# Kernel tuning notes

Hardware: AMD Instinct MI355X
Metric: run time of the kernel (lower is better)

Reference implementation:

```python
import jax, jax.numpy as jnp
import numpy as np
import math

B, L, M = 8, 1024, 1024
H, D, DK, DFF = 16, 1024, 64, 4096
EPS = 1e-5


def _ln(x, g, b):
    mu = jnp.mean(x, axis=-1, keepdims=True)
    var = jnp.mean((x - mu) ** 2, axis=-1, keepdims=True)
    return (x - mu) * jax.lax.rsqrt(var + EPS) * g + b


def _mha(x, kv, Wq, bq, Wk, bk, Wv, bv, Wo, bo, masked):
    # x: [B,Lq,D], kv: [B,Lk,D]; per-head weights stacked: Wq [H,D,DK], bq [H,DK]
    Q = jnp.einsum('bld,hdk->bhlk', x, Wq) + bq[None, :, None, :]
    K = jnp.einsum('bld,hdk->bhlk', kv, Wk) + bk[None, :, None, :]
    V = jnp.einsum('bld,hdk->bhlk', kv, Wv) + bv[None, :, None, :]
    scores = jnp.einsum('bhqk,bhmk->bhqm', Q, K) / math.sqrt(DK)
    p = jax.nn.softmax(scores, axis=-1)
    if masked:
        # faithful to source: mask applied AFTER softmax (multiply by tril ones)
        Lq = x.shape[1]
        tril = jnp.tril(jnp.ones((Lq, kv.shape[1]), dtype=p.dtype))
        p = p * tril
    z = jnp.einsum('bhqm,bhmk->bhqk', p, V)  # [B,H,Lq,DK]
    z = jnp.transpose(z, (0, 2, 1, 3)).reshape(x.shape[0], x.shape[1], H * DK)
    return z @ Wo + bo


def _forward(x, enc, Wq1, bq1, Wk1, bk1, Wv1, bv1, Wo1, bo1,
             Wq2, bq2, Wk2, bk2, Wv2, bv2, Wo2, bo2,
             W1, b1, W2, b2, g1, be1, g2, be2, g3, be3):
    z = _mha(x, x, Wq1, bq1, Wk1, bk1, Wv1, bv1, Wo1, bo1, masked=True)
    x = _ln(z + x, g1, be1)
    z = _mha(x, enc, Wq2, bq2, Wk2, bk2, Wv2, bv2, Wo2, bo2, masked=False)
    x = _ln(z + x, g2, be2)
    # Conv1d(k=1) pair == per-token MLP: relu(x @ W1 + b1) @ W2 + b2
    y = jax.nn.relu(x @ W1 + b1) @ W2 + b2
    return _ln(y + x, g3, be3)


def setup_inputs() -> dict:
    key = jax.random.key(0)
    ks = jax.random.split(key, 16)
    s = 0.02
    return {
        'x': jax.random.normal(ks[0], (B, L, D), jnp.float32),
        'enc': jax.random.normal(ks[1], (B, M, D), jnp.float32),
        'Wq1': jax.random.normal(ks[2], (H, D, DK), jnp.float32) * s,
        'bq1': jnp.zeros((H, DK), jnp.float32),
        'Wk1': jax.random.normal(ks[3], (H, D, DK), jnp.float32) * s,
        'bk1': jnp.zeros((H, DK), jnp.float32),
        'Wv1': jax.random.normal(ks[4], (H, D, DK), jnp.float32) * s,
        'bv1': jnp.zeros((H, DK), jnp.float32),
        'Wo1': jax.random.normal(ks[5], (H * DK, D), jnp.float32) * s,
        'bo1': jnp.zeros((D,), jnp.float32),
        'Wq2': jax.random.normal(ks[6], (H, D, DK), jnp.float32) * s,
        'bq2': jnp.zeros((H, DK), jnp.float32),
        'Wk2': jax.random.normal(ks[7], (H, D, DK), jnp.float32) * s,
        'bk2': jnp.zeros((H, DK), jnp.float32),
        'Wv2': jax.random.normal(ks[8], (H, D, DK), jnp.float32) * s,
        'bv2': jnp.zeros((H, DK), jnp.float32),
        'Wo2': jax.random.normal(ks[9], (H * DK, D), jnp.float32) * s,
        'bo2': jnp.zeros((D,), jnp.float32),
        'W1': jax.random.normal(ks[10], (D, DFF), jnp.float32) * s,
        'b1': jnp.zeros((DFF,), jnp.float32),
        'W2': jax.random.normal(ks[11], (DFF, D), jnp.float32) * s,
        'b2': jnp.zeros((D,), jnp.float32),
        'g1': jnp.ones((D,), jnp.float32), 'be1': jnp.zeros((D,), jnp.float32),
        'g2': jnp.ones((D,), jnp.float32), 'be2': jnp.zeros((D,), jnp.float32),
        'g3': jnp.ones((D,), jnp.float32), 'be3': jnp.zeros((D,), jnp.float32),
    }


def reference(x, enc, Wq1, bq1, Wk1, bk1, Wv1, bv1, Wo1, bo1,
              Wq2, bq2, Wk2, bk2, Wv2, bv2, Wo2, bo2,
              W1, b1, W2, b2, g1, be1, g2, be2, g3, be3):
    return _forward(x, enc, Wq1, bq1, Wk1, bk1, Wv1, bv1, Wo1, bo1,
                    Wq2, bq2, Wk2, bk2, Wv2, bv2, Wo2, bo2,
                    W1, b1, W2, b2, g1, be1, g2, be2, g3, be3)
```

## Files before the change

kernel.cpp:

```cpp
#include <hip/hip_runtime.h>
#include <hip/hip_bf16.h>

typedef __bf16 bf16;
typedef __bf16 bf16x8 __attribute__((ext_vector_type(8)));
typedef __bf16 bf16x4v __attribute__((ext_vector_type(4)));
typedef float f32x4 __attribute__((ext_vector_type(4)));
typedef unsigned int u32;
typedef u32 u32x4 __attribute__((ext_vector_type(4)));

#define DEV static __device__ __forceinline__

DEV void gll16(const void* g, void* l) {
  __builtin_amdgcn_global_load_lds((__attribute__((address_space(1))) void*)g,
                                   (__attribute__((address_space(3))) void*)l,
                                   16, 0, 0);
}

DEV bf16 tobf(float f) { return (bf16)f; }

DEV u32 cvtpk(float lo, float hi) {
  u32 r;
  asm("v_cvt_pk_bf16_f32 %0, %1, %2" : "=v"(r) : "v"(lo), "v"(hi));
  return r;
}

__global__ void cast_f2b_kernel(const float* __restrict__ in, bf16* __restrict__ out, int n4) {
  int i = blockIdx.x * 256 + threadIdx.x;
  if (i < n4) {
    const float4 v = ((const float4*)in)[i];
    bf16x4v o;
    o[0] = tobf(v.x); o[1] = tobf(v.y); o[2] = tobf(v.z); o[3] = tobf(v.w);
    ((bf16x4v*)out)[i] = o;
  }
}

__global__ __launch_bounds__(256)
void tpack_kernel(const float* __restrict__ in, bf16* __restrict__ out,
                  int K, int N, int in_hs, int out_hs, float scale) {
  __shared__ float tile[32][33];
  const int k0 = blockIdx.x << 5, n0 = blockIdx.y << 5;
  const float* ip = in + (size_t)blockIdx.z * in_hs;
  bf16* op = out + (size_t)blockIdx.z * out_hs;
  const int tx = threadIdx.x & 31, ty = threadIdx.x >> 5;
#pragma unroll
  for (int r = 0; r < 4; ++r)
    tile[ty * 4 + r][tx] = ip[(size_t)(k0 + ty * 4 + r) * N + n0 + tx];
  __syncthreads();
#pragma unroll
  for (int r = 0; r < 4; ++r)
    op[(size_t)(n0 + ty * 4 + r) * K + k0 + tx] = tobf(tile[tx][ty * 4 + r] * scale);
}

__global__ void bscale_kernel(const float* __restrict__ in, float* __restrict__ out, int n, float s) {
  int i = blockIdx.x * 256 + threadIdx.x;
  if (i < n) out[i] = in[i] * s;
}

template<int EPI>
__global__ __launch_bounds__(512, 2)
void gemm8(const bf16* __restrict__ A, const bf16* __restrict__ W,
           const float* __restrict__ bias, const float* __restrict__ resid,
           void* __restrict__ outv, int M, int N, int K) {
  __shared__ bf16 sA[3][256 * 64];
  __shared__ bf16 sB[3][128 * 64];
  const int nbx = N >> 7;
  const int nwg = (M >> 8) * nbx;
  int bid = (int)blockIdx.x;
  bid = (bid & 7) * (nwg >> 3) + (bid >> 3);
  const int tm = bid / nbx, tn = bid - tm * nbx;
  const int tid = threadIdx.x;
  const int lane = tid & 63;
  const int w = tid >> 6;
  const int wr = w >> 1, wc = w & 1;
  const int l15 = lane & 15, l4 = lane >> 4;

  const bf16* Abase = A + (size_t)(tm * 256) * K;
  const bf16* Bbase = W + (size_t)(tn * 128) * K;

  f32x4 acc[4][4] = {};
  const int nt = K >> 6;

  auto stageA = [&](int buf, int t) {
#pragma unroll
    for (int j = 0; j < 4; ++j) {
      int g = tid + (j << 9);
      int row = g >> 3;
      int sc = ((g & 7) ^ (row & 7)) << 3;
      gll16(Abase + (size_t)row * K + (t << 6) + sc, &sA[buf][g << 3]);
    }
  };
  auto stageB = [&](int buf, int t) {
#pragma unroll
    for (int j = 0; j < 2; ++j) {
      int g = tid + (j << 9);
      int row = g >> 3;
      int sc = ((g & 7) ^ (row & 7)) << 3;
      gll16(Bbase + (size_t)row * K + (t << 6) + sc, &sB[buf][g << 3]);
    }
  };

  stageA(0, 0); stageB(0, 0);
  stageA(1, 1 < nt ? 1 : 0); stageB(1, 1 < nt ? 1 : 0);
  __builtin_amdgcn_sched_barrier(0);
  asm volatile("s_waitcnt vmcnt(6)" ::: "memory");
  __builtin_amdgcn_s_barrier();

  int c = 0;
  for (int t = 0; t < nt; ++t) {
    const int sb = (c >= 1) ? c - 1 : 2;
    const int ts = (t + 2 < nt) ? t + 2 : nt - 1;
    bf16x8 af[4][2], bfr[4][2];
#pragma unroll
    for (int mi = 0; mi < 4; ++mi)
#pragma unroll
      for (int kk = 0; kk < 2; ++kk) {
        int r = wr * 64 + (mi << 4) + l15;
        int off = (r << 7) + (kk << 6) + (l4 << 4);
        off ^= (r & 7) << 4;
        af[mi][kk] = *(const bf16x8*)((const char*)sA[c] + off);
      }
#pragma unroll
    for (int ni = 0; ni < 2; ++ni)
#pragma unroll
      for (int kk = 0; kk < 2; ++kk) {
        int r = wc * 64 + (ni << 4) + l15;
        int off = (r << 7) + (kk << 6) + (l4 << 4);
        off ^= (r & 7) << 4;
        bfr[ni][kk] = *(const bf16x8*)((const char*)sB[c] + off);
      }
    stageA(sb, ts);
    __builtin_amdgcn_sched_barrier(0);
    __builtin_amdgcn_s_barrier();
    asm volatile("s_waitcnt lgkmcnt(0)" ::: "memory");
    __builtin_amdgcn_sched_barrier(0);
    __builtin_amdgcn_s_setprio(1);
#pragma unroll
    for (int mi = 0; mi < 4; ++mi)
#pragma unroll
      for (int ni = 0; ni < 2; ++ni)
#pragma unroll
        for (int kk = 0; kk < 2; ++kk)
          acc[mi][ni] = __builtin_amdgcn_mfma_f32_16x16x32_bf16(af[mi][kk], bfr[ni][kk],
                                                                acc[mi][ni], 0, 0, 0);
    __builtin_amdgcn_s_setprio(0);
    __builtin_amdgcn_sched_barrier(0);
    __builtin_amdgcn_s_barrier();
#pragma unroll
    for (int ni = 2; ni < 4; ++ni)
#pragma unroll
      for (int kk = 0; kk < 2; ++kk) {
        int r = wc * 64 + (ni << 4) + l15;
        int off = (r << 7) + (kk << 6) + (l4 << 4);
        off ^= (r & 7) << 4;
        bfr[ni][kk] = *(const bf16x8*)((const char*)sB[c] + off);
      }
    stageB(sb, ts);
    __builtin_amdgcn_sched_barrier(0);
    asm volatile("s_waitcnt vmcnt(6)" ::: "memory");
    __builtin_amdgcn_s_barrier();
    asm volatile("s_waitcnt lgkmcnt(0)" ::: "memory");
    __builtin_amdgcn_sched_barrier(0);
    __builtin_amdgcn_s_setprio(1);
#pragma unroll
    for (int mi = 0; mi < 4; ++mi)
#pragma unroll
      for (int ni = 2; ni < 4; ++ni)
#pragma unroll
        for (int kk = 0; kk < 2; ++kk)
          acc[mi][ni] = __builtin_amdgcn_mfma_f32_16x16x32_bf16(af[mi][kk], bfr[ni][kk],
                                                                acc[mi][ni], 0, 0, 0);
    __builtin_amdgcn_s_setprio(0);
    __builtin_amdgcn_sched_barrier(0);
    __builtin_amdgcn_s_barrier();
    c = (c == 2) ? 0 : c + 1;
  }

  const int row0 = tm * 256 + wr * 64 + (l4 << 2);
  const int col0 = tn * 128 + wc * 64 + l15;
#pragma unroll
  for (int ni = 0; ni < 4; ++ni) {
    const int col = col0 + (ni << 4);
    const float bv = bias ? bias[col] : 0.f;
#pragma unroll
    for (int mi = 0; mi < 4; ++mi) {
      const int rr = row0 + (mi << 4);
      f32x4 v = acc[mi][ni];
      if (EPI == 0) {
        bf16* out = (bf16*)outv;
#pragma unroll
        for (int r = 0; r < 4; ++r) out[(size_t)(rr + r) * N + col] = tobf(v[r] + bv);
      } else if (EPI == 1) {
        float* out = (float*)outv;
#pragma unroll
        for (int r = 0; r < 4; ++r) {
          size_t idx = (size_t)(rr + r) * N + col;
          out[idx] = v[r] + bv + resid[idx];
        }
      } else if (EPI == 2) {
        bf16* out = (bf16*)outv;
#pragma unroll
        for (int r = 0; r < 4; ++r) out[(size_t)(rr + r) * N + col] = tobf(fmaxf(v[r] + bv, 0.f));
      } else if (EPI == 3) {
        bf16* out = (bf16*)outv;
        const int bb = rr >> 10, l0 = rr & 1023;
        const int hh = col >> 6, dk = col & 63;
        bf16x4v pk;
#pragma unroll
        for (int r = 0; r < 4; ++r) pk[r] = tobf(v[r] + bv);
        *(bf16x4v*)(out + ((size_t)((bb * 16 + hh) * 64 + dk) << 10) + l0) = pk;
      } else {
        bf16* out = (bf16*)outv;
        const int seg = col >> 10;
        const int cc = col & 1023;
        const bool isV = (EPI == 4) ? (seg == 2) : (seg == 1);
        if (isV) {
          bf16* vout = out + (size_t)seg * 8388608;
          const int bb = rr >> 10, l0 = rr & 1023;
          const int hh = cc >> 6, dk = cc & 63;
          bf16x4v pk;
#pragma unroll
          for (int r = 0; r < 4; ++r) pk[r] = tobf(v[r] + bv);
          *(bf16x4v*)(vout + ((size_t)((bb * 16 + hh) * 64 + dk) << 10) + l0) = pk;
        } else {
          bf16* qout = out + (size_t)seg * 8388608;
#pragma unroll
          for (int r = 0; r < 4; ++r) qout[(size_t)(rr + r) * 1024 + cc] = tobf(v[r] + bv);
        }
      }
    }
  }
}

template<bool MASKED>
__global__ __launch_bounds__(256, 2)
void attn_kernel(const bf16* __restrict__ Qp, const bf16* __restrict__ Kp,
                 const bf16* __restrict__ Vt, bf16* __restrict__ Z) {
  __shared__ bf16 sK[2][64 * 64];
  __shared__ bf16 sV[2][64 * 64];
  const int Lk = 1024;
  const int d = blockIdx.x;
  const int bh = d & 127, qb = d >> 7;
  const int b = bh >> 4, h = bh & 15;
  const int q0 = qb << 7;
  const int tid = threadIdx.x, lane = tid & 63, w = tid >> 6;
  const int l15 = lane & 15, l4 = lane >> 4;

  const bf16* Qb = Qp + ((size_t)(b * 1024 + q0 + w * 32)) * 1024 + h * 64;
  bf16x8 qf[2][2];
#pragma unroll
  for (int mi = 0; mi < 2; ++mi)
#pragma unroll
    for (int kk = 0; kk < 2; ++kk)
      qf[mi][kk] = *(const bf16x8*)(Qb + (size_t)((mi << 4) + l15) * 1024 + (kk << 5) + (l4 << 3));

  f32x4 o[4][2] = {};
  float Mr[2] = {-1e30f, -1e30f}, LrP[2] = {0.f, 0.f};

  const bf16* Kb = Kp + ((size_t)b * Lk) * 1024 + h * 64;
  const bf16* Vb = Vt + ((size_t)(b * 16 + h)) * 64 * Lk;

  auto stage = [&](int buf, int t, bool withV) {
    const int kv0 = t << 6;
#pragma unroll
    for (int j = 0; j < 2; ++j) {
      int g = tid + (j << 8);
      int r = g >> 3;
      int sc = ((g & 7) ^ (r & 7)) << 3;
      gll16(Kb + (size_t)(kv0 + r) * 1024 + sc, &sK[buf][g << 3]);
      if (withV) gll16(Vb + (size_t)r * Lk + kv0 + sc, &sV[buf][g << 3]);
    }
  };
  auto needPV = [&](int t) -> bool { return !MASKED || ((t << 6) < q0 + 128); };

  const int NT = Lk >> 6;
  stage(0, 0, true);
  __syncthreads();
  int cur = 0;

  for (int t = 0; t < NT; ++t) {
    if (t + 1 < NT) stage(cur ^ 1, t + 1, needPV(t + 1));
    const int kv0 = t << 6;

    f32x4 s[4][2] = {};
#pragma unroll
    for (int n = 0; n < 4; ++n) {
      bf16x8 kf[2];
#pragma unroll
      for (int kk = 0; kk < 2; ++kk) {
        int r = (n << 4) + l15;
        int off = (r << 7) + (kk << 6) + (l4 << 4);
        off ^= (r & 7) << 4;
        kf[kk] = *(const bf16x8*)((const char*)sK[cur] + off);
      }
#pragma unroll
      for (int mi = 0; mi < 2; ++mi)
#pragma unroll
        for (int kk = 0; kk < 2; ++kk)
          s[n][mi] = __builtin_amdgcn_mfma_f32_16x16x32_bf16(kf[kk], qf[mi][kk],
                                                             s[n][mi], 0, 0, 0);
    }

#pragma unroll
    for (int mi = 0; mi < 2; ++mi) {
      float lmax = s[0][mi][0];
#pragma unroll
      for (int n = 0; n < 4; ++n)
#pragma unroll
        for (int r = 0; r < 4; ++r) lmax = fmaxf(lmax, s[n][mi][r]);
      const bool need = (t == 0) || !__all(lmax <= Mr[mi] + 8.f);
      if (need) {
        float tmx = fmaxf(lmax, __shfl_xor(lmax, 16, 64));
        tmx = fmaxf(tmx, __shfl_xor(tmx, 32, 64));
        const float Mn = fmaxf(Mr[mi], tmx);
        const float al = exp2f(Mr[mi] - Mn);
        LrP[mi] *= al;
        Mr[mi] = Mn;
#pragma unroll
        for (int r = 0; r < 4; ++r) {
          float a = __shfl(al, (l4 << 2) + r, 64);
#pragma unroll
          for (int nd = 0; nd < 4; ++nd) o[nd][mi][r] *= a;
        }
      }
      float rs = 0.f;
#pragma unroll
      for (int n = 0; n < 4; ++n)
#pragma unroll
        for (int r = 0; r < 4; ++r) {
          float p = exp2f(s[n][mi][r] - Mr[mi]);
          s[n][mi][r] = p;
          rs += p;
        }
      LrP[mi] += rs;
    }

    if (needPV(t)) {
      const bool needMask = MASKED && (kv0 + 63 > q0 + (w << 5));
      bf16x8 pa[2][2];
#pragma unroll
      for (int mi = 0; mi < 2; ++mi) {
        u32 D0[4], D1[4];
        const int qg = q0 + (w << 5) + (mi << 4) + l15;
#pragma unroll
        for (int n = 0; n < 4; ++n) {
          float pv[4];
#pragma unroll
          for (int r = 0; r < 4; ++r) {
            float p = s[n][mi][r];
            if (needMask) {
              int cg = kv0 + (n << 4) + (l4 << 2) + r;
              if (cg > qg) p = 0.f;
            }
            pv[r] = p;
          }
          D0[n] = cvtpk(pv[0], pv[1]);
          D1[n] = cvtpk(pv[2], pv[3]);
        }
        const int src = l15 + ((lane & 16) << 1);
#pragma unroll
        for (int kk = 0; kk < 2; ++kk) {
          u32 v0 = (lane & 32) ? D0[2 * kk + 1] : D0[2 * kk];
          u32 v1 = (lane & 32) ? D1[2 * kk + 1] : D1[2 * kk];
          u32x4 tw;
          tw[0] = (u32)__shfl((int)v0, src, 64);
          tw[1] = (u32)__shfl((int)v1, src, 64);
          tw[2] = (u32)__shfl((int)v0, src + 16, 64);
          tw[3] = (u32)__shfl((int)v1, src + 16, 64);
          pa[mi][kk] = __builtin_bit_cast(bf16x8, tw);
        }
      }
#pragma unroll
      for (int nd = 0; nd < 4; ++nd) {
        bf16x8 vf[2];
#pragma unroll
        for (int kk = 0; kk < 2; ++kk) {
          int r = (nd << 4) + l15;
          int off = (r << 7) + (kk << 6) + (l4 << 4);
          off ^= (r & 7) << 4;
          vf[kk] = *(const bf16x8*)((const char*)sV[cur] + off);
        }
#pragma unroll
        for (int mi = 0; mi < 2; ++mi)
#pragma unroll
          for (int kk = 0; kk < 2; ++kk)
            o[nd][mi] = __builtin_amdgcn_mfma_f32_16x16x32_bf16(pa[mi][kk], vf[kk],
                                                                o[nd][mi], 0, 0, 0);
      }
    }
    __syncthreads();
    cur ^= 1;
  }

  float inv[2][4];
#pragma unroll
  for (int mi = 0; mi < 2; ++mi) {
    float l = LrP[mi];
    l += __shfl_xor(l, 16, 64);
    l += __shfl_xor(l, 32, 64);
    const float il = 1.f / l;
#pragma unroll
    for (int r = 0; r < 4; ++r) inv[mi][r] = __shfl(il, (l4 << 2) + r, 64);
  }
  bf16* Zb = Z + ((size_t)(b * 1024 + q0 + w * 32)) * 1024 + h * 64;
#pragma unroll
  for (int nd = 0; nd < 4; ++nd)
#pragma unroll
    for (int mi = 0; mi < 2; ++mi)
#pragma unroll
      for (int r = 0; r < 4; ++r)
        Zb[(size_t)((mi << 4) + (l4 << 2) + r) * 1024 + (nd << 4) + l15] =
            tobf(o[nd][mi][r] * inv[mi][r]);
}

__global__ __launch_bounds__(256)
void ln_kernel(const float* __restrict__ in, const float* __restrict__ gw,
               const float* __restrict__ bw, float* __restrict__ outf,
               bf16* __restrict__ outb) {
  const int row = blockIdx.x, tid = threadIdx.x;
  const size_t base = (size_t)row << 10;
  const float4 v = *(const float4*)(in + base + tid * 4);
  float s = v.x + v.y + v.z + v.w;
  float ss = v.x * v.x + v.y * v.y + v.z * v.z + v.w * v.w;
#pragma unroll
  for (int d = 1; d < 64; d <<= 1) { s += __shfl_xor(s, d, 64); ss += __shfl_xor(ss, d, 64); }
  __shared__ float red[8];
  const int w = tid >> 6;
  if ((tid & 63) == 0) { red[w] = s; red[4 + w] = ss; }
  __syncthreads();
  s = red[0] + red[1] + red[2] + red[3];
  ss = red[4] + red[5] + red[6] + red[7];
  const float mu = s * (1.f / 1024.f);
  const float var = ss * (1.f / 1024.f) - mu * mu;
  const float rstd = rsqrtf(var + 1e-5f);
  const float4 g4 = *(const float4*)(gw + tid * 4);
  const float4 b4 = *(const float4*)(bw + tid * 4);
  const float o0 = (v.x - mu) * rstd * g4.x + b4.x;
  const float o1 = (v.y - mu) * rstd * g4.y + b4.y;
  const float o2 = (v.z - mu) * rstd * g4.z + b4.z;
  const float o3 = (v.w - mu) * rstd * g4.w + b4.w;
  if (outf) { float4 of; of.x = o0; of.y = o1; of.z = o2; of.w = o3;
              *(float4*)(outf + base + tid * 4) = of; }
  if (outb) { bf16x4v ob; ob[0] = tobf(o0); ob[1] = tobf(o1); ob[2] = tobf(o2); ob[3] = tobf(o3);
              *(bf16x4v*)(outb + base + tid * 4) = ob; }
}

extern "C" void kernel_launch(void* const* d_in, const int* in_sizes, int n_in,
                              void* d_out, int out_size, void* d_ws, size_t ws_size,
                              hipStream_t stream) {
  const float* x   = (const float*)d_in[0];
  const float* enc = (const float*)d_in[1];
  const float* Wq1 = (const float*)d_in[2];
  const float* bq1 = (const float*)d_in[3];
  const float* Wk1 = (const float*)d_in[4];
  const float* bk1 = (const float*)d_in[5];
  const float* Wv1 = (const float*)d_in[6];
  const float* bv1 = (const float*)d_in[7];
  const float* Wo1 = (const float*)d_in[8];
  const float* bo1 = (const float*)d_in[9];
  const float* Wq2 = (const float*)d_in[10];
  const float* bq2 = (const float*)d_in[11];
  const float* Wk2 = (const float*)d_in[12];
  const float* bk2 = (const float*)d_in[13];
  const float* Wv2 = (const float*)d_in[14];
  const float* bv2 = (const float*)d_in[15];
  const float* Wo2 = (const float*)d_in[16];
  const float* bo2 = (const float*)d_in[17];
  const float* W1  = (const float*)d_in[18];
  const float* b1  = (const float*)d_in[19];
  const float* W2  = (const float*)d_in[20];
  const float* b2  = (const float*)d_in[21];
  const float* g1  = (const float*)d_in[22];
  const float* be1 = (const float*)d_in[23];
  const float* g2  = (const float*)d_in[24];
  const float* be2 = (const float*)d_in[25];
  const float* g3  = (const float*)d_in[26];
  const float* be3 = (const float*)d_in[27];

  char* ws = (char*)d_ws;
  size_t off = 0;
  auto alloc = [&](size_t bytes) { char* p = ws + off; off += (bytes + 255) & ~(size_t)255; return p; };
  const size_t ACT = (size_t)8 * 1024 * 1024 * 2;
  const float QSC = 0.125f * 1.44269504088896f;

  bf16* xb     = (bf16*)alloc(ACT);
  bf16* encb   = (bf16*)alloc(ACT);
  bf16* Wqkv1t = (bf16*)alloc((size_t)3072 * 1024 * 2);
  bf16* Wkv2t  = (bf16*)alloc((size_t)2048 * 1024 * 2);
  bf16* Wq2t   = (bf16*)alloc((size_t)1024 * 1024 * 2);
  bf16* Wo1t   = (bf16*)alloc((size_t)1024 * 1024 * 2);
  bf16* Wo2t   = (bf16*)alloc((size_t)1024 * 1024 * 2);
  bf16* W1t    = (bf16*)alloc((size_t)4096 * 1024 * 2);
  bf16* W2t    = (bf16*)alloc((size_t)4096 * 1024 * 2);
  float* qkvb1 = (float*)alloc(3072 * 4);
  float* kvb2  = (float*)alloc(2048 * 4);
  float* sbq2  = (float*)alloc(1024 * 4);
  char*  S     = alloc((size_t)64 * 1024 * 1024);
  float* rbuf  = (float*)alloc((size_t)8 * 1024 * 1024 * 4);
  float* xnf   = (float*)alloc((size_t)8 * 1024 * 1024 * 4);
  bf16*  xnb   = (bf16*)alloc(ACT);

  bf16* q1   = (bf16*)(S);
  bf16* k1   = (bf16*)(S + ACT);
  bf16* vt1  = (bf16*)(S + 2 * ACT);
  bf16* z1   = (bf16*)(S + 3 * ACT);
  bf16* hbuf = (bf16*)S;

  dim3 b256(256);
  dim3 b512(512);
  cast_f2b_kernel<<<8192, b256, 0, stream>>>(x, xb, 2097152);
  cast_f2b_kernel<<<8192, b256, 0, stream>>>(enc, encb, 2097152);
  tpack_kernel<<<dim3(32, 2, 16), b256, 0, stream>>>(Wq1, Wqkv1t, 1024, 64, 65536, 65536, QSC);
  tpack_kernel<<<dim3(32, 2, 16), b256, 0, stream>>>(Wk1, Wqkv1t + 1048576, 1024, 64, 65536, 65536, 1.f);
  tpack_kernel<<<dim3(32, 2, 16), b256, 0, stream>>>(Wv1, Wqkv1t + 2097152, 1024, 64, 65536, 65536, 1.f);
  tpack_kernel<<<dim3(32, 2, 16), b256, 0, stream>>>(Wq2, Wq2t, 1024, 64, 65536, 65536, QSC);
  tpack_kernel<<<dim3(32, 2, 16), b256, 0, stream>>>(Wk2, Wkv2t, 1024, 64, 65536, 65536, 1.f);
  tpack_kernel<<<dim3(32, 2, 16), b256, 0, stream>>>(Wv2, Wkv2t + 1048576, 1024, 64, 65536, 65536, 1.f);
  tpack_kernel<<<dim3(32, 32, 1), b256, 0, stream>>>(Wo1, Wo1t, 1024, 1024, 0, 0, 1.f);
  tpack_kernel<<<dim3(32, 32, 1), b256, 0, stream>>>(Wo2, Wo2t, 1024, 1024, 0, 0, 1.f);
  tpack_kernel<<<dim3(32, 128, 1), b256, 0, stream>>>(W1, W1t, 1024, 4096, 0, 0, 1.f);
  tpack_kernel<<<dim3(128, 32, 1), b256, 0, stream>>>(W2, W2t, 4096, 1024, 0, 0, 1.f);
  bscale_kernel<<<4, b256, 0, stream>>>(bq1, qkvb1, 1024, QSC);
  bscale_kernel<<<4, b256, 0, stream>>>(bk1, qkvb1 + 1024, 1024, 1.f);
  bscale_kernel<<<4, b256, 0, stream>>>(bv1, qkvb1 + 2048, 1024, 1.f);
  bscale_kernel<<<4, b256, 0, stream>>>(bk2, kvb2, 1024, 1.f);
  bscale_kernel<<<4, b256, 0, stream>>>(bv2, kvb2 + 1024, 1024, 1.f);
  bscale_kernel<<<4, b256, 0, stream>>>(bq2, sbq2, 1024, QSC);

  gemm8<4><<<768, b512, 0, stream>>>(xb, Wqkv1t, qkvb1, nullptr, q1, 8192, 3072, 1024);
  attn_kernel<true><<<1024, b256, 0, stream>>>(q1, k1, vt1, z1);
  gemm8<1><<<256, b512, 0, stream>>>(z1, Wo1t, bo1, x, rbuf, 8192, 1024, 1024);
  ln_kernel<<<8192, b256, 0, stream>>>(rbuf, g1, be1, xnf, xnb);

  gemm8<0><<<256, b512, 0, stream>>>(xnb, Wq2t, sbq2, nullptr, q1, 8192, 1024, 1024);
  gemm8<5><<<512, b512, 0, stream>>>(encb, Wkv2t, kvb2, nullptr, k1, 8192, 2048, 1024);
  attn_kernel<false><<<1024, b256, 0, stream>>>(q1, k1, vt1, z1);
  gemm8<1><<<256, b512, 0, stream>>>(z1, Wo2t, bo2, xnf, rbuf, 8192, 1024, 1024);
  ln_kernel<<<8192, b256, 0, stream>>>(rbuf, g2, be2, xnf, xnb);

  gemm8<2><<<1024, b512, 0, stream>>>(xnb, W1t, b1, nullptr, hbuf, 8192, 4096, 1024);
  gemm8<1><<<256, b512, 0, stream>>>(hbuf, W2t, b2, xnf, rbuf, 8192, 1024, 4096);
  ln_kernel<<<8192, b256, 0, stream>>>(rbuf, g3, be3, (float*)d_out, nullptr);
}
```

Measured before the change: 603.3 us.

## Compute V projections as transposed GEMMs and group GEMM tiles for locality

```diff
diff --git a/kernel.cpp b/kernel.cpp
--- a/kernel.cpp
+++ b/kernel.cpp
@@ -9,6 +9,11 @@
 typedef u32 u32x4 __attribute__((ext_vector_type(4)));
 
 #define DEV static __device__ __forceinline__
+#define SB0 __builtin_amdgcn_sched_barrier(0)
+#define BAR __builtin_amdgcn_s_barrier()
+#define LGKM0 asm volatile("s_waitcnt lgkmcnt(0)" ::: "memory")
+#define PRIO1 __builtin_amdgcn_s_setprio(1)
+#define PRIO0 __builtin_amdgcn_s_setprio(0)
 
 DEV void gll16(const void* g, void* l) {
   __builtin_amdgcn_global_load_lds((__attribute__((address_space(1))) void*)g,
@@ -56,8 +61,20 @@
   if (i < n) out[i] = in[i] * s;
 }
 
+DEV void tile_map(int bid, int nwg, int nbx, int& tm, int& tn) {
+  bid = (bid & 7) * (nwg >> 3) + (bid >> 3);
+  const int gid = bid >> 4, g4 = bid & 15;
+  const int gpr = nbx >> 2;
+  tm = ((gid / gpr) << 2) | (g4 >> 2);
+  tn = ((gid % gpr) << 2) | (g4 & 3);
+}
+
+DEV int lane_base(int l15, int l4, int kk) {
+  return (l15 << 7) + (((kk << 6) | (l4 << 4)) ^ ((l15 & 7) << 4));
+}
+
 template<int EPI>
-__global__ __launch_bounds__(512, 2)
+__global__ __launch_bounds__(512, 1)
 void gemm8(const bf16* __restrict__ A, const bf16* __restrict__ W,
            const float* __restrict__ bias, const float* __restrict__ resid,
            void* __restrict__ outv, int M, int N, int K) {
@@ -65,9 +82,8 @@
   __shared__ bf16 sB[3][128 * 64];
   const int nbx = N >> 7;
   const int nwg = (M >> 8) * nbx;
-  int bid = (int)blockIdx.x;
-  bid = (bid & 7) * (nwg >> 3) + (bid >> 3);
-  const int tm = bid / nbx, tn = bid - tm * nbx;
+  int tm, tn;
+  tile_map((int)blockIdx.x, nwg, nbx, tm, tn);
   const int tid = threadIdx.x;
   const int lane = tid & 63;
   const int w = tid >> 6;
@@ -77,63 +93,74 @@
   const bf16* Abase = A + (size_t)(tm * 256) * K;
   const bf16* Bbase = W + (size_t)(tn * 128) * K;
 
+  const bf16* gAsrc[4];
+  int loffA[4];
+#pragma unroll
+  for (int j = 0; j < 4; ++j) {
+    int g = tid + (j << 9);
+    int row = g >> 3;
+    int sc = ((g & 7) ^ (row & 7)) << 3;
+    gAsrc[j] = Abase + (size_t)row * K + sc;
+    loffA[j] = g << 4;
+  }
+  const bf16* gBsrc[2];
+  int loffB[2];
+#pragma unroll
+  for (int j = 0; j < 2; ++j) {
+    int g = tid + (j << 9);
+    int row = g >> 3;
+    int sc = ((g & 7) ^ (row & 7)) << 3;
+    gBsrc[j] = Bbase + (size_t)row * K + sc;
+    loffB[j] = g << 4;
+  }
+
+  int obA[2], obB[2];
+#pragma unroll
+  for (int kk = 0; kk < 2; ++kk) {
+    obA[kk] = wr * 8192 + lane_base(l15, l4, kk);
+    obB[kk] = wc * 8192 + lane_base(l15, l4, kk);
+  }
+
   f32x4 acc[4][4] = {};
   const int nt = K >> 6;
 
   auto stageA = [&](int buf, int t) {
-#pragma unroll
-    for (int j = 0; j < 4; ++j) {
-      int g = tid + (j << 9);
-      int row = g >> 3;
-      int sc = ((g & 7) ^ (row & 7)) << 3;
-      gll16(Abase + (size_t)row * K + (t << 6) + sc, &sA[buf][g << 3]);
-    }
+    const int db = buf << 15;
+    const size_t so = (size_t)t << 6;
+#pragma unroll
+    for (int j = 0; j < 4; ++j) gll16(gAsrc[j] + so, (char*)sA + db + loffA[j]);
   };
   auto stageB = [&](int buf, int t) {
-#pragma unroll
-    for (int j = 0; j < 2; ++j) {
-      int g = tid + (j << 9);
-      int row = g >> 3;
-      int sc = ((g & 7) ^ (row & 7)) << 3;
-      gll16(Bbase + (size_t)row * K + (t << 6) + sc, &sB[buf][g << 3]);
-    }
+    const int db = buf << 14;
+    const size_t so = (size_t)t << 6;
+#pragma unroll
+    for (int j = 0; j < 2; ++j) gll16(gBsrc[j] + so, (char*)sB + db + loffB[j]);
   };
 
   stageA(0, 0); stageB(0, 0);
   stageA(1, 1 < nt ? 1 : 0); stageB(1, 1 < nt ? 1 : 0);
-  __builtin_amdgcn_sched_barrier(0);
+  SB0;
   asm volatile("s_waitcnt vmcnt(6)" ::: "memory");
-  __builtin_amdgcn_s_barrier();
+  BAR;
 
   int c = 0;
   for (int t = 0; t < nt; ++t) {
     const int sb = (c >= 1) ? c - 1 : 2;
     const int ts = (t + 2 < nt) ? t + 2 : nt - 1;
+    const int aOff = c << 15, bOff = c << 14;
     bf16x8 af[4][2], bfr[4][2];
 #pragma unroll
     for (int mi = 0; mi < 4; ++mi)
 #pragma unroll
-      for (int kk = 0; kk < 2; ++kk) {
-        int r = wr * 64 + (mi << 4) + l15;
-        int off = (r << 7) + (kk << 6) + (l4 << 4);
-        off ^= (r & 7) << 4;
-        af[mi][kk] = *(const bf16x8*)((const char*)sA[c] + off);
-      }
+      for (int kk = 0; kk < 2; ++kk)
+        af[mi][kk] = *(const bf16x8*)((const char*)sA + aOff + obA[kk] + (mi << 11));
 #pragma unroll
     for (int ni = 0; ni < 2; ++ni)
 #pragma unroll
-      for (int kk = 0; kk < 2; ++kk) {
-        int r = wc * 64 + (ni << 4) + l15;
-        int off = (r << 7) + (kk << 6) + (l4 << 4);
-        off ^= (r & 7) << 4;
-        bfr[ni][kk] = *(const bf16x8*)((const char*)sB[c] + off);
-      }
+      for (int kk = 0; kk < 2; ++kk)
+        bfr[ni][kk] = *(const bf16x8*)((const char*)sB + bOff + obB[kk] + (ni << 11));
     stageA(sb, ts);
-    __builtin_amdgcn_sched_barrier(0);
-    __builtin_amdgcn_s_barrier();
-    asm volatile("s_waitcnt lgkmcnt(0)" ::: "memory");
-    __builtin_amdgcn_sched_barrier(0);
-    __builtin_amdgcn_s_setprio(1);
+    SB0; BAR; LGKM0; SB0; PRIO1;
 #pragma unroll
     for (int mi = 0; mi < 4; ++mi)
 #pragma unroll
@@ -142,25 +169,16 @@
         for (int kk = 0; kk < 2; ++kk)
           acc[mi][ni] = __builtin_amdgcn_mfma_f32_16x16x32_bf16(af[mi][kk], bfr[ni][kk],
                                                                 acc[mi][ni], 0, 0, 0);
-    __builtin_amdgcn_s_setprio(0);
-    __builtin_amdgcn_sched_barrier(0);
-    __builtin_amdgcn_s_barrier();
+    PRIO0; SB0; BAR;
 #pragma unroll
     for (int ni = 2; ni < 4; ++ni)
 #pragma unroll
-      for (int kk = 0; kk < 2; ++kk) {
-        int r = wc * 64 + (ni << 4) + l15;
-        int off = (r << 7) + (kk << 6) + (l4 << 4);
-        off ^= (r & 7) << 4;
-        bfr[ni][kk] = *(const bf16x8*)((const char*)sB[c] + off);
-      }
+      for (int kk = 0; kk < 2; ++kk)
+        bfr[ni][kk] = *(const bf16x8*)((const char*)sB + bOff + obB[kk] + (ni << 11));
     stageB(sb, ts);
-    __builtin_amdgcn_sched_barrier(0);
+    SB0;
     asm volatile("s_waitcnt vmcnt(6)" ::: "memory");
-    __builtin_amdgcn_s_barrier();
-    asm volatile("s_waitcnt lgkmcnt(0)" ::: "memory");
-    __builtin_amdgcn_sched_barrier(0);
-    __builtin_amdgcn_s_setprio(1);
+    BAR; LGKM0; SB0; PRIO1;
 #pragma unroll
     for (int mi = 0; mi < 4; ++mi)
 #pragma unroll
@@ -169,9 +187,7 @@
         for (int kk = 0; kk < 2; ++kk)
           acc[mi][ni] = __builtin_amdgcn_mfma_f32_16x16x32_bf16(af[mi][kk], bfr[ni][kk],
                                                                 acc[mi][ni], 0, 0, 0);
-    __builtin_amdgcn_s_setprio(0);
-    __builtin_amdgcn_sched_barrier(0);
-    __builtin_amdgcn_s_barrier();
+    PRIO0; SB0; BAR;
     c = (c == 2) ? 0 : c + 1;
   }
 
@@ -180,7 +196,7 @@
 #pragma unroll
   for (int ni = 0; ni < 4; ++ni) {
     const int col = col0 + (ni << 4);
-    const float bv = bias ? bias[col] : 0.f;
+    const float bv = (EPI == 6) ? 0.f : bias[col];
 #pragma unroll
     for (int mi = 0; mi < 4; ++mi) {
       const int rr = row0 + (mi << 4);
@@ -200,32 +216,19 @@
         bf16* out = (bf16*)outv;
 #pragma unroll
         for (int r = 0; r < 4; ++r) out[(size_t)(rr + r) * N + col] = tobf(fmaxf(v[r] + bv, 0.f));
-      } else if (EPI == 3) {
-        bf16* out = (bf16*)outv;
-        const int bb = rr >> 10, l0 = rr & 1023;
-        const int hh = col >> 6, dk = col & 63;
-        bf16x4v pk;
-#pragma unroll
-        for (int r = 0; r < 4; ++r) pk[r] = tobf(v[r] + bv);
-        *(bf16x4v*)(out + ((size_t)((bb * 16 + hh) * 64 + dk) << 10) + l0) = pk;
-      } else {
+      } else if (EPI == 4) {
         bf16* out = (bf16*)outv;
         const int seg = col >> 10;
         const int cc = col & 1023;
-        const bool isV = (EPI == 4) ? (seg == 2) : (seg == 1);
-        if (isV) {
-          bf16* vout = out + (size_t)seg * 8388608;
-          const int bb = rr >> 10, l0 = rr & 1023;
-          const int hh = cc >> 6, dk = cc & 63;
-          bf16x4v pk;
-#pragma unroll
-          for (int r = 0; r < 4; ++r) pk[r] = tobf(v[r] + bv);
-          *(bf16x4v*)(vout + ((size_t)((bb * 16 + hh) * 64 + dk) << 10) + l0) = pk;
-        } else {
-          bf16* qout = out + (size_t)seg * 8388608;
-#pragma unroll
-          for (int r = 0; r < 4; ++r) qout[(size_t)(rr + r) * 1024 + cc] = tobf(v[r] + bv);
-        }
+        bf16* qout = out + (size_t)seg * 8388608;
+#pragma unroll
+        for (int r = 0; r < 4; ++r) qout[(size_t)(rr + r) * 1024 + cc] = tobf(v[r] + bv);
+      } else {
+        bf16* out = (bf16*)outv;
+        const float4 bq = *(const float4*)(bias + rr);
+        const float br[4] = {bq.x, bq.y, bq.z, bq.w};
+#pragma unroll
+        for (int r = 0; r < 4; ++r) out[(size_t)(rr + r) * N + col] = tobf(v[r] + br[r]);
       }
     }
   }
@@ -257,7 +260,7 @@
   float Mr[2] = {-1e30f, -1e30f}, LrP[2] = {0.f, 0.f};
 
   const bf16* Kb = Kp + ((size_t)b * Lk) * 1024 + h * 64;
-  const bf16* Vb = Vt + ((size_t)(b * 16 + h)) * 64 * Lk;
+  const bf16* Vb = Vt + (size_t)(h * 64) * 8192 + b * 1024;
 
   auto stage = [&](int buf, int t, bool withV) {
     const int kv0 = t << 6;
@@ -267,7 +270,7 @@
       int r = g >> 3;
       int sc = ((g & 7) ^ (r & 7)) << 3;
       gll16(Kb + (size_t)(kv0 + r) * 1024 + sc, &sK[buf][g << 3]);
-      if (withV) gll16(Vb + (size_t)r * Lk + kv0 + sc, &sV[buf][g << 3]);
+      if (withV) gll16(Vb + (size_t)r * 8192 + kv0 + sc, &sV[buf][g << 3]);
     }
   };
   auto needPV = [&](int t) -> bool { return !MASKED || ((t << 6) < q0 + 128); };
@@ -484,15 +487,16 @@
 
   bf16* xb     = (bf16*)alloc(ACT);
   bf16* encb   = (bf16*)alloc(ACT);
-  bf16* Wqkv1t = (bf16*)alloc((size_t)3072 * 1024 * 2);
-  bf16* Wkv2t  = (bf16*)alloc((size_t)2048 * 1024 * 2);
+  bf16* Wqk1t  = (bf16*)alloc((size_t)2048 * 1024 * 2);
+  bf16* Wv1t   = (bf16*)alloc((size_t)1024 * 1024 * 2);
   bf16* Wq2t   = (bf16*)alloc((size_t)1024 * 1024 * 2);
+  bf16* Wk2t   = (bf16*)alloc((size_t)1024 * 1024 * 2);
+  bf16* Wv2t   = (bf16*)alloc((size_t)1024 * 1024 * 2);
   bf16* Wo1t   = (bf16*)alloc((size_t)1024 * 1024 * 2);
   bf16* Wo2t   = (bf16*)alloc((size_t)1024 * 1024 * 2);
   bf16* W1t    = (bf16*)alloc((size_t)4096 * 1024 * 2);
   bf16* W2t    = (bf16*)alloc((size_t)4096 * 1024 * 2);
-  float* qkvb1 = (float*)alloc(3072 * 4);
-  float* kvb2  = (float*)alloc(2048 * 4);
+  float* qkb1  = (float*)alloc(2048 * 4);
   float* sbq2  = (float*)alloc(1024 * 4);
   char*  S     = alloc((size_t)64 * 1024 * 1024);
   float* rbuf  = (float*)alloc((size_t)8 * 1024 * 1024 * 4);
@@ -509,30 +513,29 @@
   dim3 b512(512);
   cast_f2b_kernel<<<8192, b256, 0, stream>>>(x, xb, 2097152);
   cast_f2b_kernel<<<8192, b256, 0, stream>>>(enc, encb, 2097152);
-  tpack_kernel<<<dim3(32, 2, 16), b256, 0, stream>>>(Wq1, Wqkv1t, 1024, 64, 65536, 65536, QSC);
-  tpack_kernel<<<dim3(32, 2, 16), b256, 0, stream>>>(Wk1, Wqkv1t + 1048576, 1024, 64, 65536, 65536, 1.f);
-  tpack_kernel<<<dim3(32, 2, 16), b256, 0, stream>>>(Wv1, Wqkv1t + 2097152, 1024, 64, 65536, 65536, 1.f);
+  tpack_kernel<<<dim3(32, 2, 16), b256, 0, stream>>>(Wq1, Wqk1t, 1024, 64, 65536, 65536, QSC);
+  tpack_kernel<<<dim3(32, 2, 16), b256, 0, stream>>>(Wk1, Wqk1t + 1048576, 1024, 64, 65536, 65536, 1.f);
+  tpack_kernel<<<dim3(32, 2, 16), b256, 0, stream>>>(Wv1, Wv1t, 1024, 64, 65536, 65536, 1.f);
   tpack_kernel<<<dim3(32, 2, 16), b256, 0, stream>>>(Wq2, Wq2t, 1024, 64, 65536, 65536, QSC);
-  tpack_kernel<<<dim3(32, 2, 16), b256, 0, stream>>>(Wk2, Wkv2t, 1024, 64, 65536, 65536, 1.f);
-  tpack_kernel<<<dim3(32, 2, 16), b256, 0, stream>>>(Wv2, Wkv2t + 1048576, 1024, 64, 65536, 65536, 1.f);
+  tpack_kernel<<<dim3(32, 2, 16), b256, 0, stream>>>(Wk2, Wk2t, 1024, 64, 65536, 65536, 1.f);
+  tpack_kernel<<<dim3(32, 2, 16), b256, 0, stream>>>(Wv2, Wv2t, 1024, 64, 65536, 65536, 1.f);
   tpack_kernel<<<dim3(32, 32, 1), b256, 0, stream>>>(Wo1, Wo1t, 1024, 1024, 0, 0, 1.f);
   tpack_kernel<<<dim3(32, 32, 1), b256, 0, stream>>>(Wo2, Wo2t, 1024, 1024, 0, 0, 1.f);
   tpack_kernel<<<dim3(32, 128, 1), b256, 0, stream>>>(W1, W1t, 1024, 4096, 0, 0, 1.f);
   tpack_kernel<<<dim3(128, 32, 1), b256, 0, stream>>>(W2, W2t, 4096, 1024, 0, 0, 1.f);
-  bscale_kernel<<<4, b256, 0, stream>>>(bq1, qkvb1, 1024, QSC);
-  bscale_kernel<<<4, b256, 0, stream>>>(bk1, qkvb1 + 1024, 1024, 1.f);
-  bscale_kernel<<<4, b256, 0, stream>>>(bv1, qkvb1 + 2048, 1024, 1.f);
-  bscale_kernel<<<4, b256, 0, stream>>>(bk2, kvb2, 1024, 1.f);
-  bscale_kernel<<<4, b256, 0, stream>>>(bv2, kvb2 + 1024, 1024, 1.f);
+  bscale_kernel<<<4, b256, 0, stream>>>(bq1, qkb1, 1024, QSC);
+  bscale_kernel<<<4, b256, 0, stream>>>(bk1, qkb1 + 1024, 1024, 1.f);
   bscale_kernel<<<4, b256, 0, stream>>>(bq2, sbq2, 1024, QSC);
 
-  gemm8<4><<<768, b512, 0, stream>>>(xb, Wqkv1t, qkvb1, nullptr, q1, 8192, 3072, 1024);
+  gemm8<4><<<512, b512, 0, stream>>>(xb, Wqk1t, qkb1, nullptr, q1, 8192, 2048, 1024);
+  gemm8<6><<<256, b512, 0, stream>>>(Wv1t, xb, bv1, nullptr, vt1, 1024, 8192, 1024);
   attn_kernel<true><<<1024, b256, 0, stream>>>(q1, k1, vt1, z1);
   gemm8<1><<<256, b512, 0, stream>>>(z1, Wo1t, bo1, x, rbuf, 8192, 1024, 1024);
   ln_kernel<<<8192, b256, 0, stream>>>(rbuf, g1, be1, xnf, xnb);
 
   gemm8<0><<<256, b512, 0, stream>>>(xnb, Wq2t, sbq2, nullptr, q1, 8192, 1024, 1024);
-  gemm8<5><<<512, b512, 0, stream>>>(encb, Wkv2t, kvb2, nullptr, k1, 8192, 2048, 1024);
+  gemm8<0><<<256, b512, 0, stream>>>(encb, Wk2t, bk2, nullptr, k1, 8192, 1024, 1024);
+  gemm8<6><<<256, b512, 0, stream>>>(Wv2t, encb, bv2, nullptr, vt1, 1024, 8192, 1024);
   attn_kernel<false><<<1024, b256, 0, stream>>>(q1, k1, vt1, z1);
   gemm8<1><<<256, b512, 0, stream>>>(z1, Wo2t, bo2, xnf, rbuf, 8192, 1024, 1024);
   ln_kernel<<<8192, b256, 0, stream>>>(rbuf, g2, be2, xnf, xnb);
```

Result: no change. 595.3 us (-1.3%).
